# Performance work log

Hardware: AMD Instinct MI355X
Metric: run time of the kernel (lower is better)

## Reference

```python
import jax, jax.numpy as jnp
import numpy as np

N_NODES = 50000
N_EDGES = 800000
IN_DIM = 256
HID = [256, 128]
NEG_SLOPE = 0.01  # F.leaky_relu default


def setup_inputs() -> dict:
    key = jax.random.key(0)
    ks = jax.random.split(key, 8)
    x = jax.random.normal(ks[0], (N_NODES, IN_DIM), dtype=jnp.float32)
    w1 = jax.random.normal(ks[1], (IN_DIM, HID[0]), dtype=jnp.float32) * (1.0 / np.sqrt(IN_DIM))
    b1 = jnp.zeros((HID[0],), dtype=jnp.float32)
    w2 = jax.random.normal(ks[2], (HID[0], HID[1]), dtype=jnp.float32) * (1.0 / np.sqrt(HID[0]))
    b2 = jnp.zeros((HID[1],), dtype=jnp.float32)
    src = jax.random.randint(ks[3], (N_EDGES,), 0, N_NODES, dtype=jnp.int32)
    dst = jax.random.randint(ks[4], (N_EDGES,), 0, N_NODES, dtype=jnp.int32)
    edge_weight = jax.random.uniform(ks[5], (N_EDGES,), dtype=jnp.float32)
    return {"x": x, "w1": w1, "b1": b1, "w2": w2, "b2": b2,
            "src": src, "dst": dst, "edge_weight": edge_weight}


def _gcn_layer(h, w, b, src, dst, ew, n_nodes):
    # GraphConvolution: support = h @ W ; out = spmm(adj, support) + b
    support = h @ w                              # [N, d_out]
    msg = support[src] * ew[:, None]             # [E, d_out] gather + scale
    agg = jax.ops.segment_sum(msg, dst, num_segments=n_nodes)  # [N, d_out]
    return agg + b


def reference(x, w1, b1, w2, b2, src, dst, edge_weight):
    # layer 1: GCN -> leaky_relu -> dropout(eval: identity)
    h = _gcn_layer(x, w1, b1, src, dst, edge_weight, N_NODES)
    h = jax.nn.leaky_relu(h, NEG_SLOPE)
    # layer 2
    h = _gcn_layer(h, w2, b2, src, dst, edge_weight, N_NODES)
    h = jax.nn.leaky_relu(h, NEG_SLOPE)
    return h
```

## Files before the change

kernel.cpp:

```cpp
#include <hip/hip_runtime.h>

#define NEG_SLOPE 0.01f

constexpr int N_NODES_C = 50000;
constexpr int N_EDGES_C = 800000;
constexpr int M_PAD = 50048;

typedef short bf16x8 __attribute__((ext_vector_type(8)));
typedef float f32x4 __attribute__((ext_vector_type(4)));

__device__ inline unsigned short f2bf(float f) {
  unsigned int u = __float_as_uint(f);
  u += 0x7FFF + ((u >> 16) & 1);
  return (unsigned short)(u >> 16);
}
__device__ inline float bf2f(unsigned int h16) {
  return __uint_as_float(h16 << 16);
}

constexpr int NB_CONVX = (M_PAD * 32) / 256;
constexpr int NB_W1 = (256 * 256) / 256;
constexpr int NB_W2 = (256 * 128) / 256;
constexpr int NB_HIST = ((N_EDGES_C / 4) + 255) / 256;
constexpr int NB_PRE = NB_CONVX + NB_W1 + NB_W2 + NB_HIST;

__global__ __launch_bounds__(256) void pre_kernel(
    const float* __restrict__ x, const float* __restrict__ w1,
    const float* __restrict__ w2, const int* __restrict__ dst,
    unsigned short* __restrict__ xb, unsigned short* __restrict__ w1T,
    unsigned short* __restrict__ w2T, int* __restrict__ counts) {
  const int bx = blockIdx.x;
  const int tid = threadIdx.x;
  if (bx < NB_CONVX) {
    int idx = bx * 256 + tid;
    int row = idx >> 5;
    int c8 = (idx & 31) << 3;
    uint4 v;
    if (row < N_NODES_C) {
      const float4* p = (const float4*)(x + (size_t)row * 256 + c8);
      float4 a = p[0], b = p[1];
      v.x = f2bf(a.x) | ((unsigned)f2bf(a.y) << 16);
      v.y = f2bf(a.z) | ((unsigned)f2bf(a.w) << 16);
      v.z = f2bf(b.x) | ((unsigned)f2bf(b.y) << 16);
      v.w = f2bf(b.z) | ((unsigned)f2bf(b.w) << 16);
    } else {
      v = make_uint4(0, 0, 0, 0);
    }
    *(uint4*)(xb + (size_t)row * 256 + c8) = v;
  } else if (bx < NB_CONVX + NB_W1) {
    int idx = (bx - NB_CONVX) * 256 + tid;
    int n = idx >> 8, k = idx & 255;
    w1T[idx] = f2bf(w1[(size_t)k * 256 + n]);
  } else if (bx < NB_CONVX + NB_W1 + NB_W2) {
    int idx = (bx - NB_CONVX - NB_W1) * 256 + tid;
    int n = idx >> 8, k = idx & 255;
    w2T[idx] = f2bf(w2[(size_t)k * 128 + n]);
  } else {
    int g = (bx - NB_CONVX - NB_W1 - NB_W2) * 256 + tid;
    int e = g * 4;
    if (e < N_EDGES_C) {
      int4 d4 = *(const int4*)(dst + e);
      atomicAdd(&counts[d4.x], 1);
      atomicAdd(&counts[d4.y], 1);
      atomicAdd(&counts[d4.z], 1);
      atomicAdd(&counts[d4.w], 1);
    }
  }
}

constexpr int N_SCAN_BLKS = (N_NODES_C + 255) / 256;

__global__ __launch_bounds__(256) void scan_phase_a(const int* __restrict__ counts,
                                                    int* __restrict__ partial,
                                                    int* __restrict__ blk_sums) {
  __shared__ int s[256];
  const int t = threadIdx.x;
  const int i = blockIdx.x * 256 + t;
  const int v = (i < N_NODES_C) ? counts[i] : 0;
  s[t] = v;
  __syncthreads();
  for (int off = 1; off < 256; off <<= 1) {
    int u = (t >= off) ? s[t - off] : 0;
    __syncthreads();
    s[t] += u;
    __syncthreads();
  }
  if (i < N_NODES_C) partial[i] = s[t] - v;
  if (t == 255) blk_sums[blockIdx.x] = s[255];
}

__global__ __launch_bounds__(256) void scan_phase_bc(const int* __restrict__ partial,
                                                     const int* __restrict__ blk_sums,
                                                     int* __restrict__ row_ptr,
                                                     int* __restrict__ cursor) {
  __shared__ int s[256];
  __shared__ int blk_excl;
  const int t = threadIdx.x;
  const int v = (t < N_SCAN_BLKS) ? blk_sums[t] : 0;
  s[t] = v;
  __syncthreads();
  for (int off = 1; off < 256; off <<= 1) {
    int u = (t >= off) ? s[t - off] : 0;
    __syncthreads();
    s[t] += u;
    __syncthreads();
  }
  if (t == (int)blockIdx.x) blk_excl = s[t] - v;
  __syncthreads();
  const int i = blockIdx.x * 256 + t;
  if (i < N_NODES_C) {
    const int r = partial[i] + blk_excl;
    row_ptr[i] = r;
    cursor[i] = r;
  }
  if (i == 0) row_ptr[N_NODES_C] = N_EDGES_C;
}


#define GLOAD_LDS16(g, l)                                              \
  __builtin_amdgcn_global_load_lds(                                    \
      (__attribute__((address_space(1))) void*)(g),                    \
      (__attribute__((address_space(3))) void*)(l), 16, 0, 0)

__device__ __forceinline__ void gemm_tile(
    const unsigned short* __restrict__ A,
    const unsigned short* __restrict__ BT,
    unsigned short* __restrict__ C,
    int N, int row0, int col0, short* Asm, short* Bsm) {
  constexpr int K = 256;
  const int tid = threadIdx.x;
  const int lane = tid & 63, wave = tid >> 6;
  const int wm = wave & 1, wn = wave >> 1;

  const int ch0 = wave * 2, ch1 = wave * 2 + 1;
  const int o0 = ch0 * 512 + lane * 8;
  const int o1 = ch1 * 512 + lane * 8;
  const int r0 = o0 >> 5, c0 = o0 & 31;
  const int r1 = o1 >> 5, c1 = o1 & 31;

  f32x4 acc[4][4] = {};

  for (int k0 = 0; k0 < K; k0 += 32) {
    GLOAD_LDS16(A + (size_t)(row0 + r0) * K + k0 + c0, &Asm[ch0 * 512]);
    GLOAD_LDS16(A + (size_t)(row0 + r1) * K + k0 + c1, &Asm[ch1 * 512]);
    GLOAD_LDS16(BT + (size_t)(col0 + r0) * K + k0 + c0, &Bsm[ch0 * 512]);
    GLOAD_LDS16(BT + (size_t)(col0 + r1) * K + k0 + c1, &Bsm[ch1 * 512]);
    __builtin_amdgcn_s_waitcnt(0);
    __syncthreads();

    bf16x8 af[4], bf[4];
#pragma unroll
    for (int mt = 0; mt < 4; ++mt)
      af[mt] = *(const bf16x8*)&Asm[(wm * 64 + mt * 16 + (lane & 15)) * 32 + (lane >> 4) * 8];
#pragma unroll
    for (int nt = 0; nt < 4; ++nt)
      bf[nt] = *(const bf16x8*)&Bsm[(wn * 64 + nt * 16 + (lane & 15)) * 32 + (lane >> 4) * 8];
#pragma unroll
    for (int mt = 0; mt < 4; ++mt)
#pragma unroll
      for (int nt = 0; nt < 4; ++nt)
        acc[mt][nt] = __builtin_amdgcn_mfma_f32_16x16x32_bf16(af[mt], bf[nt], acc[mt][nt], 0, 0, 0);
    __syncthreads();
  }

  const int cl = lane & 15, rq = (lane >> 4) * 4;
#pragma unroll
  for (int mt = 0; mt < 4; ++mt) {
    const int rbase = row0 + wm * 64 + mt * 16 + rq;
#pragma unroll
    for (int nt = 0; nt < 4; ++nt) {
      const int col = col0 + wn * 64 + nt * 16 + cl;
      const size_t sbase = ((size_t)(col >> 5) * M_PAD) * 32 + (col & 31);
#pragma unroll
      for (int i = 0; i < 4; ++i)
        C[sbase + (size_t)(rbase + i) * 32] = f2bf(acc[mt][nt][i]);
    }
  }
}

constexpr int NB_GEMM1 = 2 * (M_PAD / 128);
constexpr int NB_FILL = ((N_EDGES_C / 4) + 255) / 256;

__global__ __launch_bounds__(256) void fill_gemm1_kernel(
    const unsigned short* __restrict__ A, const unsigned short* __restrict__ BT,
    unsigned short* __restrict__ C, const int* __restrict__ src,
    const int* __restrict__ dst, const float* __restrict__ ew,
    int* __restrict__ cursor, unsigned* __restrict__ s_meta) {
  __shared__ short Asm[128 * 32];
  __shared__ short Bsm[128 * 32];
  const int b = blockIdx.x;
  if ((b & 1) == 0) {
    const int t = b >> 1;
    gemm_tile(A, BT, C, 256, (t >> 1) * 128, (t & 1) * 128, Asm, Bsm);
  } else {
    const int g = (b >> 1) * 256 + threadIdx.x;
    const int e = g * 4;
    if (e < N_EDGES_C) {
      int4 d4 = *(const int4*)(dst + e);
      int4 s4 = *(const int4*)(src + e);
      float4 w4 = *(const float4*)(ew + e);
      unsigned m0 = (unsigned)s4.x | ((unsigned)f2bf(w4.x) << 16);
      unsigned m1 = (unsigned)s4.y | ((unsigned)f2bf(w4.y) << 16);
      unsigned m2 = (unsigned)s4.z | ((unsigned)f2bf(w4.z) << 16);
      unsigned m3 = (unsigned)s4.w | ((unsigned)f2bf(w4.w) << 16);
      int p0 = atomicAdd(&cursor[d4.x], 1);
      int p1 = atomicAdd(&cursor[d4.y], 1);
      int p2 = atomicAdd(&cursor[d4.z], 1);
      int p3 = atomicAdd(&cursor[d4.w], 1);
      __builtin_nontemporal_store(m0, s_meta + p0);
      __builtin_nontemporal_store(m1, s_meta + p1);
      __builtin_nontemporal_store(m2, s_meta + p2);
      __builtin_nontemporal_store(m3, s_meta + p3);
    }
  }
}

__global__ __launch_bounds__(256) void gemm2_kernel(
    const unsigned short* __restrict__ A, const unsigned short* __restrict__ BT,
    unsigned short* __restrict__ C) {
  __shared__ short Asm[128 * 32];
  __shared__ short Bsm[128 * 32];
  gemm_tile(A, BT, C, 128, blockIdx.x * 128, 0, Asm, Bsm);
}


__device__ inline void fma8(float* acc, uint4 v, float wt) {
  acc[0] += bf2f(v.x & 0xffffu) * wt;
  acc[1] += bf2f(v.x >> 16) * wt;
  acc[2] += bf2f(v.y & 0xffffu) * wt;
  acc[3] += bf2f(v.y >> 16) * wt;
  acc[4] += bf2f(v.z & 0xffffu) * wt;
  acc[5] += bf2f(v.z >> 16) * wt;
  acc[6] += bf2f(v.w & 0xffffu) * wt;
  acc[7] += bf2f(v.w >> 16) * wt;
}

template <int NSLICE, int OUT_D, bool OUT_BF16>
__global__ __launch_bounds__(64) void agg_lite_kernel(
    const unsigned short* __restrict__ supS,
    const unsigned* __restrict__ s_meta,
    const int* __restrict__ row_ptr, const float* __restrict__ bias,
    unsigned short* __restrict__ out_bf, float* __restrict__ out_f, int n_total) {
  const int bx = blockIdx.x;
  const int slice = bx & (NSLICE - 1);
  const int group = bx / NSLICE;
  const int lane = threadIdx.x;
  const int quad = lane >> 2;
  const int dimg = lane & 3;
  const int n = group * 16 + quad;
  if (n >= n_total) return;
  const bool valid = n < N_NODES_C;
  const unsigned short* tab = supS + (size_t)slice * M_PAD * 32;

  float acc[8] = {};
  if (valid) {
    int j = row_ptr[n];
    const int end = row_ptr[n + 1];
    for (; j + 2 <= end; j += 2) {
      unsigned m0 = s_meta[j];
      unsigned m1 = s_meta[j + 1];
      uint4 v0 = *(const uint4*)(tab + (m0 & 0xffffu) * 32 + dimg * 8);
      uint4 v1 = *(const uint4*)(tab + (m1 & 0xffffu) * 32 + dimg * 8);
      fma8(acc, v0, bf2f(m0 >> 16));
      fma8(acc, v1, bf2f(m1 >> 16));
    }
    if (j < end) {
      unsigned m0 = s_meta[j];
      uint4 v0 = *(const uint4*)(tab + (m0 & 0xffffu) * 32 + dimg * 8);
      fma8(acc, v0, bf2f(m0 >> 16));
    }
  }

  const int dbase = slice * 32 + dimg * 8;
  if (OUT_BF16) {
    unsigned short o[8];
#pragma unroll
    for (int j = 0; j < 8; ++j) {
      if (valid) {
        float v = acc[j] + bias[dbase + j];
        v = v >= 0.f ? v : NEG_SLOPE * v;
        o[j] = f2bf(v);
      } else {
        o[j] = 0;
      }
    }
    uint4 pk;
    pk.x = o[0] | ((unsigned)o[1] << 16);
    pk.y = o[2] | ((unsigned)o[3] << 16);
    pk.z = o[4] | ((unsigned)o[5] << 16);
    pk.w = o[6] | ((unsigned)o[7] << 16);
    *(uint4*)(out_bf + (size_t)n * OUT_D + dbase) = pk;
  } else if (valid) {
    float r[8];
#pragma unroll
    for (int j = 0; j < 8; ++j) {
      float v = acc[j] + bias[dbase + j];
      r[j] = v >= 0.f ? v : NEG_SLOPE * v;
    }
    *(float4*)(out_f + (size_t)n * OUT_D + dbase) = make_float4(r[0], r[1], r[2], r[3]);
    *(float4*)(out_f + (size_t)n * OUT_D + dbase + 4) = make_float4(r[4], r[5], r[6], r[7]);
  }
}


extern "C" void kernel_launch(void* const* d_in, const int* in_sizes, int n_in,
                              void* d_out, int out_size, void* d_ws, size_t ws_size,
                              hipStream_t stream) {
  const float* x  = (const float*)d_in[0];
  const float* w1 = (const float*)d_in[1];
  const float* b1 = (const float*)d_in[2];
  const float* w2 = (const float*)d_in[3];
  const float* b2 = (const float*)d_in[4];
  const int*   src = (const int*)d_in[5];
  const int*   dst = (const int*)d_in[6];
  const float* ew  = (const float*)d_in[7];
  float* out = (float*)d_out;

  unsigned short* xb   = (unsigned short*)d_ws;
  unsigned short* a2b  = xb + (size_t)M_PAD * 256;
  unsigned short* sup1 = a2b + (size_t)M_PAD * 256;
  unsigned short* sup2 = sup1 + (size_t)M_PAD * 256;
  unsigned short* w1T  = sup2 + (size_t)M_PAD * 128;
  unsigned short* w2T  = w1T + 256 * 256;
  int* counts  = (int*)(w2T + 128 * 256);
  int* cursor  = counts + N_NODES_C;
  int* row_ptr = cursor + N_NODES_C;
  int* partial = row_ptr + (N_NODES_C + 1);
  int* blk_sums= partial + N_NODES_C;
  unsigned* s_meta = (unsigned*)(blk_sums + 256);

  hipMemsetAsync(counts, 0, N_NODES_C * sizeof(int), stream);
  pre_kernel<<<NB_PRE, 256, 0, stream>>>(x, w1, w2, dst, xb, w1T, w2T, counts);

  scan_phase_a<<<N_SCAN_BLKS, 256, 0, stream>>>(counts, partial, blk_sums);
  scan_phase_bc<<<N_SCAN_BLKS, 256, 0, stream>>>(partial, blk_sums, row_ptr, cursor);

  fill_gemm1_kernel<<<NB_GEMM1 + NB_FILL, 256, 0, stream>>>(
      xb, w1T, sup1, src, dst, ew, cursor, s_meta);

  agg_lite_kernel<8, 256, true><<<(M_PAD / 16) * 8, 64, 0, stream>>>(
      sup1, s_meta, row_ptr, b1, a2b, nullptr, M_PAD);

  gemm2_kernel<<<M_PAD / 128, 256, 0, stream>>>(a2b, w2T, sup2);
  agg_lite_kernel<4, 128, false><<<(N_NODES_C / 16) * 4, 64, 0, stream>>>(
      sup2, s_meta, row_ptr, b2, nullptr, out, N_NODES_C);
}
```

Baseline: 301.8 us.

## Sort nodes by in-degree to balance aggregation work and unroll edge loop by four

Adds a degree histogram in the scan and a counting-sort pass fused into the fill/GEMM1 launch that builds a permutation of nodes grouped by in-degree. The aggregation kernels then process nodes in permuted order, so the 16 nodes sharing a wavefront have similar edge counts and lanes diverge less. The edge loop is also unrolled from two to four gathers to raise memory-level parallelism. This costs extra histogram atomics, a perm array read per node, and scattered output writes in the aggregation kernels.

Result: no change. 306.5 us (+1.6%).

```diff
diff --git a/kernel.cpp b/kernel.cpp
--- a/kernel.cpp
+++ b/kernel.cpp
@@ -72,12 +72,15 @@
 
 __global__ __launch_bounds__(256) void scan_phase_a(const int* __restrict__ counts,
                                                     int* __restrict__ partial,
-                                                    int* __restrict__ blk_sums) {
+                                                    int* __restrict__ blk_sums,
+                                                    int* __restrict__ hist2) {
   __shared__ int s[256];
+  __shared__ int lh[64];
   const int t = threadIdx.x;
   const int i = blockIdx.x * 256 + t;
   const int v = (i < N_NODES_C) ? counts[i] : 0;
   s[t] = v;
+  if (t < 64) lh[t] = 0;
   __syncthreads();
   for (int off = 1; off < 256; off <<= 1) {
     int u = (t >= off) ? s[t - off] : 0;
@@ -85,14 +88,24 @@
     s[t] += u;
     __syncthreads();
   }
-  if (i < N_NODES_C) partial[i] = s[t] - v;
+  if (i < N_NODES_C) {
+    partial[i] = s[t] - v;
+    atomicAdd(&lh[v < 63 ? v : 63], 1);
+  }
   if (t == 255) blk_sums[blockIdx.x] = s[255];
+  __syncthreads();
+  if (t < 64) {
+    int c = lh[t];
+    if (c) atomicAdd(&hist2[t], c);
+  }
 }
 
 __global__ __launch_bounds__(256) void scan_phase_bc(const int* __restrict__ partial,
                                                      const int* __restrict__ blk_sums,
                                                      int* __restrict__ row_ptr,
-                                                     int* __restrict__ cursor) {
+                                                     int* __restrict__ cursor,
+                                                     const int* __restrict__ hist2,
+                                                     int* __restrict__ cursor2) {
   __shared__ int s[256];
   __shared__ int blk_excl;
   const int t = threadIdx.x;
@@ -114,6 +127,16 @@
     cursor[i] = r;
   }
   if (i == 0) row_ptr[N_NODES_C] = N_EDGES_C;
+  if (blockIdx.x == 0 && t < 64) {
+    int hv = hist2[t];
+    int x = hv;
+#pragma unroll
+    for (int off = 1; off < 64; off <<= 1) {
+      int u = __shfl_up(x, off);
+      if (t >= off) x += u;
+    }
+    cursor2[t] = x - hv;
+  }
 }
 
 
@@ -180,38 +203,65 @@
 
 constexpr int NB_GEMM1 = 2 * (M_PAD / 128);
 constexpr int NB_FILL = ((N_EDGES_C / 4) + 255) / 256;
+constexpr int NB_SCAT = (M_PAD + 255) / 256;
 
 __global__ __launch_bounds__(256) void fill_gemm1_kernel(
     const unsigned short* __restrict__ A, const unsigned short* __restrict__ BT,
     unsigned short* __restrict__ C, const int* __restrict__ src,
     const int* __restrict__ dst, const float* __restrict__ ew,
-    int* __restrict__ cursor, unsigned* __restrict__ s_meta) {
+    int* __restrict__ cursor, unsigned* __restrict__ s_meta,
+    const int* __restrict__ counts, int* __restrict__ cursor2,
+    int* __restrict__ perm) {
   __shared__ short Asm[128 * 32];
   __shared__ short Bsm[128 * 32];
+  __shared__ int lhist[64];
+  __shared__ int lbase[64];
   const int b = blockIdx.x;
-  if ((b & 1) == 0) {
-    const int t = b >> 1;
-    gemm_tile(A, BT, C, 256, (t >> 1) * 128, (t & 1) * 128, Asm, Bsm);
+  if (b < NB_GEMM1 + NB_FILL) {
+    if ((b & 1) == 0) {
+      const int t = b >> 1;
+      gemm_tile(A, BT, C, 256, (t >> 1) * 128, (t & 1) * 128, Asm, Bsm);
+    } else {
+      const int g = (b >> 1) * 256 + threadIdx.x;
+      const int e = g * 4;
+      if (e < N_EDGES_C) {
+        int4 d4 = *(const int4*)(dst + e);
+        int4 s4 = *(const int4*)(src + e);
+        float4 w4 = *(const float4*)(ew + e);
+        unsigned m0 = (unsigned)s4.x | ((unsigned)f2bf(w4.x) << 16);
+        unsigned m1 = (unsigned)s4.y | ((unsigned)f2bf(w4.y) << 16);
+        unsigned m2 = (unsigned)s4.z | ((unsigned)f2bf(w4.z) << 16);
+        unsigned m3 = (unsigned)s4.w | ((unsigned)f2bf(w4.w) << 16);
+        int p0 = atomicAdd(&cursor[d4.x], 1);
+        int p1 = atomicAdd(&cursor[d4.y], 1);
+        int p2 = atomicAdd(&cursor[d4.z], 1);
+        int p3 = atomicAdd(&cursor[d4.w], 1);
+        __builtin_nontemporal_store(m0, s_meta + p0);
+        __builtin_nontemporal_store(m1, s_meta + p1);
+        __builtin_nontemporal_store(m2, s_meta + p2);
+        __builtin_nontemporal_store(m3, s_meta + p3);
+      }
+    }
   } else {
-    const int g = (b >> 1) * 256 + threadIdx.x;
-    const int e = g * 4;
-    if (e < N_EDGES_C) {
-      int4 d4 = *(const int4*)(dst + e);
-      int4 s4 = *(const int4*)(src + e);
-      float4 w4 = *(const float4*)(ew + e);
-      unsigned m0 = (unsigned)s4.x | ((unsigned)f2bf(w4.x) << 16);
-      unsigned m1 = (unsigned)s4.y | ((unsigned)f2bf(w4.y) << 16);
-      unsigned m2 = (unsigned)s4.z | ((unsigned)f2bf(w4.z) << 16);
-      unsigned m3 = (unsigned)s4.w | ((unsigned)f2bf(w4.w) << 16);
-      int p0 = atomicAdd(&cursor[d4.x], 1);
-      int p1 = atomicAdd(&cursor[d4.y], 1);
-      int p2 = atomicAdd(&cursor[d4.z], 1);
-      int p3 = atomicAdd(&cursor[d4.w], 1);
-      __builtin_nontemporal_store(m0, s_meta + p0);
-      __builtin_nontemporal_store(m1, s_meta + p1);
-      __builtin_nontemporal_store(m2, s_meta + p2);
-      __builtin_nontemporal_store(m3, s_meta + p3);
-    }
+    const int t = threadIdx.x;
+    if (t < 64) lhist[t] = 0;
+    __syncthreads();
+    const int idx = (b - NB_GEMM1 - NB_FILL) * 256 + t;
+    int d = -1, lrank = 0;
+    if (idx < N_NODES_C) {
+      d = counts[idx];
+      if (d > 63) d = 63;
+      lrank = atomicAdd(&lhist[d], 1);
+    } else if (idx < M_PAD) {
+      perm[idx] = idx;
+    }
+    __syncthreads();
+    if (t < 64) {
+      int c = lhist[t];
+      lbase[t] = c ? atomicAdd(&cursor2[t], c) : 0;
+    }
+    __syncthreads();
+    if (d >= 0) perm[lbase[d] + lrank] = idx;
   }
 }
 
@@ -240,6 +290,7 @@
     const unsigned short* __restrict__ supS,
     const unsigned* __restrict__ s_meta,
     const int* __restrict__ row_ptr, const float* __restrict__ bias,
+    const int* __restrict__ perm,
     unsigned short* __restrict__ out_bf, float* __restrict__ out_f, int n_total) {
   const int bx = blockIdx.x;
   const int slice = bx & (NSLICE - 1);
@@ -247,8 +298,9 @@
   const int lane = threadIdx.x;
   const int quad = lane >> 2;
   const int dimg = lane & 3;
-  const int n = group * 16 + quad;
-  if (n >= n_total) return;
+  const int idx = group * 16 + quad;
+  if (idx >= n_total) return;
+  const int n = perm[idx];
   const bool valid = n < N_NODES_C;
   const unsigned short* tab = supS + (size_t)slice * M_PAD * 32;
 
@@ -256,15 +308,21 @@
   if (valid) {
     int j = row_ptr[n];
     const int end = row_ptr[n + 1];
-    for (; j + 2 <= end; j += 2) {
+    for (; j + 4 <= end; j += 4) {
       unsigned m0 = s_meta[j];
       unsigned m1 = s_meta[j + 1];
+      unsigned m2 = s_meta[j + 2];
+      unsigned m3 = s_meta[j + 3];
       uint4 v0 = *(const uint4*)(tab + (m0 & 0xffffu) * 32 + dimg * 8);
       uint4 v1 = *(const uint4*)(tab + (m1 & 0xffffu) * 32 + dimg * 8);
+      uint4 v2 = *(const uint4*)(tab + (m2 & 0xffffu) * 32 + dimg * 8);
+      uint4 v3 = *(const uint4*)(tab + (m3 & 0xffffu) * 32 + dimg * 8);
       fma8(acc, v0, bf2f(m0 >> 16));
       fma8(acc, v1, bf2f(m1 >> 16));
-    }
-    if (j < end) {
+      fma8(acc, v2, bf2f(m2 >> 16));
+      fma8(acc, v3, bf2f(m3 >> 16));
+    }
+    for (; j < end; ++j) {
       unsigned m0 = s_meta[j];
       uint4 v0 = *(const uint4*)(tab + (m0 & 0xffffu) * 32 + dimg * 8);
       fma8(acc, v0, bf2f(m0 >> 16));
@@ -328,20 +386,25 @@
   int* partial = row_ptr + (N_NODES_C + 1);
   int* blk_sums= partial + N_NODES_C;
   unsigned* s_meta = (unsigned*)(blk_sums + 256);
+  int* hist2   = (int*)(s_meta + N_EDGES_C);
+  int* cursor2 = hist2 + 64;
+  int* perm    = cursor2 + 64;
 
   hipMemsetAsync(counts, 0, N_NODES_C * sizeof(int), stream);
+  hipMemsetAsync(hist2, 0, 64 * sizeof(int), stream);
   pre_kernel<<<NB_PRE, 256, 0, stream>>>(x, w1, w2, dst, xb, w1T, w2T, counts);
 
-  scan_phase_a<<<N_SCAN_BLKS, 256, 0, stream>>>(counts, partial, blk_sums);
-  scan_phase_bc<<<N_SCAN_BLKS, 256, 0, stream>>>(partial, blk_sums, row_ptr, cursor);
-
-  fill_gemm1_kernel<<<NB_GEMM1 + NB_FILL, 256, 0, stream>>>(
-      xb, w1T, sup1, src, dst, ew, cursor, s_meta);
+  scan_phase_a<<<N_SCAN_BLKS, 256, 0, stream>>>(counts, partial, blk_sums, hist2);
+  scan_phase_bc<<<N_SCAN_BLKS, 256, 0, stream>>>(partial, blk_sums, row_ptr, cursor,
+                                                 hist2, cursor2);
+
+  fill_gemm1_kernel<<<NB_GEMM1 + NB_FILL + NB_SCAT, 256, 0, stream>>>(
+      xb, w1T, sup1, src, dst, ew, cursor, s_meta, counts, cursor2, perm);
 
   agg_lite_kernel<8, 256, true><<<(M_PAD / 16) * 8, 64, 0, stream>>>(
-      sup1, s_meta, row_ptr, b1, a2b, nullptr, M_PAD);
+      sup1, s_meta, row_ptr, b1, perm, a2b, nullptr, M_PAD);
 
   gemm2_kernel<<<M_PAD / 128, 256, 0, stream>>>(a2b, w2T, sup2);
   agg_lite_kernel<4, 128, false><<<(N_NODES_C / 16) * 4, 64, 0, stream>>>(
-      sup2, s_meta, row_ptr, b2, nullptr, out, N_NODES_C);
-}
+      sup2, s_meta, row_ptr, b2, perm, nullptr, out, N_NODES_C);
+}
```

## Sort nodes by degree and pad edge lists to quads for aggregation

Applied to the files above, without the earlier changes.

Replaces the CSR prefix scan with a degree-histogram counting sort. Nodes are bucketed by in-degree (capped at 63), and each node's edge segment is padded to a multiple of four with zero-weight entries. Aggregation then visits nodes in degree order, so the 16 nodes in a block have similar work, and it reads metadata as uint4 with four gathers issued per step. The goal is to cut intra-wave load imbalance and meta-load latency, at the cost of a permutation indirection, extra padded edges and less locality in output writes.

New measurement: 287.6 us. -4.7%, faster.

```diff
diff --git a/kernel.cpp b/kernel.cpp
--- a/kernel.cpp
+++ b/kernel.cpp
@@ -5,6 +5,7 @@
 constexpr int N_NODES_C = 50000;
 constexpr int N_EDGES_C = 800000;
 constexpr int M_PAD = 50048;
+constexpr int META_CAP = 950016;
 
 typedef short bf16x8 __attribute__((ext_vector_type(8)));
 typedef float f32x4 __attribute__((ext_vector_type(4)));
@@ -68,52 +69,81 @@
   }
 }
 
-constexpr int N_SCAN_BLKS = (N_NODES_C + 255) / 256;
-
-__global__ __launch_bounds__(256) void scan_phase_a(const int* __restrict__ counts,
-                                                    int* __restrict__ partial,
-                                                    int* __restrict__ blk_sums) {
-  __shared__ int s[256];
+constexpr int NB_NODE = (N_NODES_C + 255) / 256;
+constexpr int NB_SCAT = (M_PAD + 255) / 256;
+
+__global__ __launch_bounds__(256) void hist_kernel(const int* __restrict__ counts,
+                                                   int* __restrict__ hist2,
+                                                   int* __restrict__ ehist) {
+  __shared__ int lh[64], le[64];
   const int t = threadIdx.x;
-  const int i = blockIdx.x * 256 + t;
-  const int v = (i < N_NODES_C) ? counts[i] : 0;
-  s[t] = v;
-  __syncthreads();
-  for (int off = 1; off < 256; off <<= 1) {
-    int u = (t >= off) ? s[t - off] : 0;
-    __syncthreads();
-    s[t] += u;
-    __syncthreads();
-  }
-  if (i < N_NODES_C) partial[i] = s[t] - v;
-  if (t == 255) blk_sums[blockIdx.x] = s[255];
-}
-
-__global__ __launch_bounds__(256) void scan_phase_bc(const int* __restrict__ partial,
-                                                     const int* __restrict__ blk_sums,
-                                                     int* __restrict__ row_ptr,
-                                                     int* __restrict__ cursor) {
-  __shared__ int s[256];
-  __shared__ int blk_excl;
-  const int t = threadIdx.x;
-  const int v = (t < N_SCAN_BLKS) ? blk_sums[t] : 0;
-  s[t] = v;
-  __syncthreads();
-  for (int off = 1; off < 256; off <<= 1) {
-    int u = (t >= off) ? s[t - off] : 0;
-    __syncthreads();
-    s[t] += u;
-    __syncthreads();
-  }
-  if (t == (int)blockIdx.x) blk_excl = s[t] - v;
+  if (t < 64) { lh[t] = 0; le[t] = 0; }
   __syncthreads();
   const int i = blockIdx.x * 256 + t;
   if (i < N_NODES_C) {
-    const int r = partial[i] + blk_excl;
-    row_ptr[i] = r;
-    cursor[i] = r;
-  }
-  if (i == 0) row_ptr[N_NODES_C] = N_EDGES_C;
+    int d = counts[i];
+    int bin = d < 63 ? d : 63;
+    atomicAdd(&lh[bin], 1);
+    atomicAdd(&le[bin], (d + 3) & ~3);
+  }
+  __syncthreads();
+  if (t < 64) {
+    if (lh[t]) atomicAdd(&hist2[t], lh[t]);
+    if (le[t]) atomicAdd(&ehist[t], le[t]);
+  }
+}
+
+__global__ __launch_bounds__(256) void scatter_kernel(
+    const int* __restrict__ counts, const int* __restrict__ hist2,
+    const int* __restrict__ ehist, int* __restrict__ gclaim_n,
+    int* __restrict__ gclaim_e, int* __restrict__ perm,
+    int* __restrict__ nstart, int* __restrict__ ndeg,
+    int* __restrict__ cursor, unsigned* __restrict__ s_meta) {
+  __shared__ int nbase[64], ebase[64], lh[64], le[64], gn[64], ge[64];
+  const int t = threadIdx.x;
+  if (t < 64) {
+    int hv = hist2[t], ev = ehist[t];
+    int xs = hv, xe = ev;
+#pragma unroll
+    for (int off = 1; off < 64; off <<= 1) {
+      int a = __shfl_up(xs, off);
+      int b = __shfl_up(xe, off);
+      if (t >= off) { xs += a; xe += b; }
+    }
+    nbase[t] = xs - hv;
+    ebase[t] = xe - ev;
+    lh[t] = 0;
+    le[t] = 0;
+  }
+  __syncthreads();
+  const int idx = blockIdx.x * 256 + t;
+  int d = -1, bin = 0, lrank = 0, erank = 0;
+  if (idx < N_NODES_C) {
+    d = counts[idx];
+    bin = d < 63 ? d : 63;
+    lrank = atomicAdd(&lh[bin], 1);
+    erank = atomicAdd(&le[bin], (d + 3) & ~3);
+  } else if (idx < M_PAD) {
+    perm[idx] = idx;
+    nstart[idx] = 0;
+    ndeg[idx] = 0;
+  }
+  __syncthreads();
+  if (t < 64) {
+    gn[t] = lh[t] ? nbase[t] + atomicAdd(&gclaim_n[t], lh[t]) : 0;
+    ge[t] = le[t] ? ebase[t] + atomicAdd(&gclaim_e[t], le[t]) : 0;
+  }
+  __syncthreads();
+  if (d >= 0) {
+    const int grank = gn[bin] + lrank;
+    const int estart = ge[bin] + erank;
+    perm[grank] = idx;
+    nstart[grank] = estart;
+    ndeg[grank] = d;
+    cursor[idx] = estart;
+    const int d4 = (d + 3) & ~3;
+    for (int j = d; j < d4; ++j) s_meta[estart + j] = 0;
+  }
 }
 
 
@@ -235,11 +265,25 @@
   acc[7] += bf2f(v.w >> 16) * wt;
 }
 
+__device__ __forceinline__ void gfma4(float* acc, uint4 m,
+                                      const unsigned short* __restrict__ tab,
+                                      int dimg) {
+  uint4 v0 = *(const uint4*)(tab + (m.x & 0xffffu) * 32 + dimg * 8);
+  uint4 v1 = *(const uint4*)(tab + (m.y & 0xffffu) * 32 + dimg * 8);
+  uint4 v2 = *(const uint4*)(tab + (m.z & 0xffffu) * 32 + dimg * 8);
+  uint4 v3 = *(const uint4*)(tab + (m.w & 0xffffu) * 32 + dimg * 8);
+  fma8(acc, v0, bf2f(m.x >> 16));
+  fma8(acc, v1, bf2f(m.y >> 16));
+  fma8(acc, v2, bf2f(m.z >> 16));
+  fma8(acc, v3, bf2f(m.w >> 16));
+}
+
 template <int NSLICE, int OUT_D, bool OUT_BF16>
 __global__ __launch_bounds__(64) void agg_lite_kernel(
     const unsigned short* __restrict__ supS,
     const unsigned* __restrict__ s_meta,
-    const int* __restrict__ row_ptr, const float* __restrict__ bias,
+    const int* __restrict__ nstart, const int* __restrict__ ndeg,
+    const int* __restrict__ perm, const float* __restrict__ bias,
     unsigned short* __restrict__ out_bf, float* __restrict__ out_f, int n_total) {
   const int bx = blockIdx.x;
   const int slice = bx & (NSLICE - 1);
@@ -247,28 +291,31 @@
   const int lane = threadIdx.x;
   const int quad = lane >> 2;
   const int dimg = lane & 3;
-  const int n = group * 16 + quad;
-  if (n >= n_total) return;
+  const int idx = group * 16 + quad;
+  if (idx >= n_total) return;
+  const int n = perm[idx];
   const bool valid = n < N_NODES_C;
   const unsigned short* tab = supS + (size_t)slice * M_PAD * 32;
 
   float acc[8] = {};
-  if (valid) {
-    int j = row_ptr[n];
-    const int end = row_ptr[n + 1];
-    for (; j + 2 <= end; j += 2) {
-      unsigned m0 = s_meta[j];
-      unsigned m1 = s_meta[j + 1];
-      uint4 v0 = *(const uint4*)(tab + (m0 & 0xffffu) * 32 + dimg * 8);
-      uint4 v1 = *(const uint4*)(tab + (m1 & 0xffffu) * 32 + dimg * 8);
-      fma8(acc, v0, bf2f(m0 >> 16));
-      fma8(acc, v1, bf2f(m1 >> 16));
-    }
-    if (j < end) {
-      unsigned m0 = s_meta[j];
-      uint4 v0 = *(const uint4*)(tab + (m0 & 0xffffu) * 32 + dimg * 8);
-      fma8(acc, v0, bf2f(m0 >> 16));
-    }
+  const int s = nstart[idx];
+  const int nq = (ndeg[idx] + 3) >> 2;
+  const uint4* mp = (const uint4*)(s_meta + s);
+
+  if (nq > 0) {
+    uint4 m0 = mp[0];
+    uint4 m1 = (nq > 1) ? mp[1] : make_uint4(0, 0, 0, 0);
+    int q = 0;
+    for (; q + 2 < nq; q += 2) {
+      uint4 p0 = mp[q + 2];
+      uint4 p1 = mp[q + 3];
+      gfma4(acc, m0, tab, dimg);
+      gfma4(acc, m1, tab, dimg);
+      m0 = p0;
+      m1 = p1;
+    }
+    gfma4(acc, m0, tab, dimg);
+    if (q + 1 < nq) gfma4(acc, m1, tab, dimg);
   }
 
   const int dbase = slice * 32 + dimg * 8;
@@ -324,24 +371,31 @@
   unsigned short* w2T  = w1T + 256 * 256;
   int* counts  = (int*)(w2T + 128 * 256);
   int* cursor  = counts + N_NODES_C;
-  int* row_ptr = cursor + N_NODES_C;
-  int* partial = row_ptr + (N_NODES_C + 1);
-  int* blk_sums= partial + N_NODES_C;
-  unsigned* s_meta = (unsigned*)(blk_sums + 256);
+  int* perm    = cursor + N_NODES_C;
+  int* nstart  = perm + M_PAD;
+  int* ndeg    = nstart + M_PAD;
+  int* hist2   = ndeg + M_PAD;
+  int* ehist   = hist2 + 64;
+  int* gclaim_n= ehist + 64;
+  int* gclaim_e= gclaim_n + 64;
+  unsigned* s_meta = (unsigned*)(gclaim_e + 64);
 
   hipMemsetAsync(counts, 0, N_NODES_C * sizeof(int), stream);
+  hipMemsetAsync(hist2, 0, 256 * sizeof(int), stream);
   pre_kernel<<<NB_PRE, 256, 0, stream>>>(x, w1, w2, dst, xb, w1T, w2T, counts);
 
-  scan_phase_a<<<N_SCAN_BLKS, 256, 0, stream>>>(counts, partial, blk_sums);
-  scan_phase_bc<<<N_SCAN_BLKS, 256, 0, stream>>>(partial, blk_sums, row_ptr, cursor);
+  hist_kernel<<<NB_NODE, 256, 0, stream>>>(counts, hist2, ehist);
+  scatter_kernel<<<NB_SCAT, 256, 0, stream>>>(counts, hist2, ehist, gclaim_n,
+                                              gclaim_e, perm, nstart, ndeg,
+                                              cursor, s_meta);
 
   fill_gemm1_kernel<<<NB_GEMM1 + NB_FILL, 256, 0, stream>>>(
       xb, w1T, sup1, src, dst, ew, cursor, s_meta);
 
   agg_lite_kernel<8, 256, true><<<(M_PAD / 16) * 8, 64, 0, stream>>>(
-      sup1, s_meta, row_ptr, b1, a2b, nullptr, M_PAD);
+      sup1, s_meta, nstart, ndeg, perm, b1, a2b, nullptr, M_PAD);
 
   gemm2_kernel<<<M_PAD / 128, 256, 0, stream>>>(a2b, w2T, sup2);
   agg_lite_kernel<4, 128, false><<<(N_NODES_C / 16) * 4, 64, 0, stream>>>(
-      sup2, s_meta, row_ptr, b2, nullptr, out, N_NODES_C);
-}
+      sup2, s_meta, nstart, ndeg, perm, b2, nullptr, out, N_NODES_C);
+}
```
